# Performance work log

Hardware: AMD Instinct MI355X
Metric: run time of the kernel (lower is better)

The kernel has to match this reference:

```python
import jax, jax.numpy as jnp
import numpy as np

N, E, C, K = 50000, 800000, 64, 8
D = C * K  # 512
NEG_SLOPE = 0.01  # torch leaky_relu default


def setup_inputs() -> dict:
    key = jax.random.key(0)
    ks = jax.random.split(key, 6)
    x = jax.random.normal(ks[0], (N, D), dtype=jnp.float32)
    edge_index = jax.random.randint(ks[1], (2, E), 0, N, dtype=jnp.int64)
    conv_W = jax.random.normal(ks[2], (K, C, C), dtype=jnp.float32) * (1.0 / np.sqrt(C))
    conv_b = jax.random.normal(ks[3], (K, C), dtype=jnp.float32) * 0.01
    W1 = jax.random.normal(ks[4], (D, D), dtype=jnp.float32) * (1.0 / np.sqrt(D))
    W2 = jax.random.normal(ks[5], (D, D), dtype=jnp.float32) * (1.0 / np.sqrt(D))
    return {"x": x, "edge_index": edge_index, "conv_W": conv_W,
            "conv_b": conv_b, "W1": W1, "W2": W2}


def _gcn_conv(xk, Wk, bk, src, dst, dinv, n):
    # PyG GCNConv: transform, then symmetric-normalized aggregation with self-loops,
    # then add bias.
    xt = xk @ Wk.T  # [N, C]
    norm = dinv[src] * dinv[dst]  # [E]
    agg = jax.ops.segment_sum(norm[:, None] * xt[src], dst, num_segments=n)
    agg = agg + (dinv * dinv)[:, None] * xt  # self-loop contribution
    return agg + bk


def reference(x, edge_index, conv_W, conv_b, W1, W2):
    n = x.shape[0]
    src, dst = edge_index[0], edge_index[1]
    # degree with self-loops (edge weight 1)
    deg = jax.ops.segment_sum(jnp.ones((E,), x.dtype), dst, num_segments=n) + 1.0
    dinv = deg ** -0.5
    xr = x.reshape(n, C, K)
    zs = [jax.nn.leaky_relu(_gcn_conv(xr[:, :, i], conv_W[i], conv_b[i], src, dst, dinv, n),
                            negative_slope=NEG_SLOPE)
          for i in range(K)]
    z = jnp.concatenate(zs, axis=1)  # [N, D]
    z = jax.nn.leaky_relu(z, negative_slope=NEG_SLOPE)
    # dropout is identity in eval mode (dr=12 is invalid for torch Dropout anyway)
    z_fc1 = z @ W1.T
    z_fc2 = z @ W2.T
    s = jnp.sum(z_fc1.T @ z_fc2, axis=0)  # [D]
    # softmax over axis 0 of a [1, D] tensor (as in the original code)
    gate = jax.nn.softmax((s / jnp.sqrt(jnp.asarray(D, x.dtype)))[None, :], axis=0)
    return z * gate
```

## Files before the change

kernel.cpp:

```cpp
#include <hip/hip_runtime.h>

#define NN 50000
#define EE 800000
#define KK 8
#define DD 512
#define CAP 64
#define TR_BLOCKS   ((NN + 31) / 32)
#define FILL_BLOCKS ((EE + 255) / 256)
#define LROW 520

typedef __attribute__((ext_vector_type(8))) short short8;
typedef __attribute__((ext_vector_type(4))) float f32x4;
typedef __attribute__((ext_vector_type(4))) unsigned u32x4;

__device__ __forceinline__ float leaky2(float v) {
    v = (v < 0.0f) ? 0.01f * v : v;
    v = (v < 0.0f) ? 0.01f * v : v;
    return v;
}

__device__ __forceinline__ unsigned short f2bf(float f) {
    unsigned u = __float_as_uint(f);
    u += 0x7fffu + ((u >> 16) & 1u);
    return (unsigned short)(u >> 16);
}
__device__ __forceinline__ float bf_lo(unsigned u) { return __uint_as_float(u << 16); }
__device__ __forceinline__ float bf_hi(unsigned u) { return __uint_as_float(u & 0xffff0000u); }

__device__ __forceinline__ void fma8(float acc[8], float w, u32x4 v) {
    acc[0] += w * bf_lo(v[0]); acc[1] += w * bf_hi(v[0]);
    acc[2] += w * bf_lo(v[1]); acc[3] += w * bf_hi(v[1]);
    acc[4] += w * bf_lo(v[2]); acc[5] += w * bf_hi(v[2]);
    acc[6] += w * bf_lo(v[3]); acc[7] += w * bf_hi(v[3]);
}

__global__ __launch_bounds__(256) void k_fill_transform(
        const int* __restrict__ ei, int* __restrict__ cursor,
        unsigned short* __restrict__ bw,
        const float* __restrict__ x, const float* __restrict__ W,
        unsigned short* __restrict__ xt) {
    __shared__ unsigned short lxT[32 * LROW];
    const int t = threadIdx.x;

    if (blockIdx.x >= TR_BLOCKS) {
        int e = (blockIdx.x - TR_BLOCKS) * 256 + t;
        if (e < EE) {
            int s = ei[e];
            int d = ei[EE + e];
            int p = atomicAdd(&cursor[d], 1);
            if (p < CAP) bw[(size_t)d * CAP + p] = (unsigned short)s;
        }
        return;
    }

    const int n0 = blockIdx.x * 32;

    const f32x4* x4 = (const f32x4*)x;
    #pragma unroll
    for (int i = 0; i < 16; i++) {
        int idx = i * 256 + t;
        int n = idx >> 7;
        int q = idx & 127;
        int n_eff = n0 + n; if (n_eff >= NN) n_eff = NN - 1;
        f32x4 v = __builtin_nontemporal_load(&x4[(size_t)n_eff * 128 + q]);
        int c = q >> 1;
        int k0 = (q & 1) * 4;
        unsigned short* p = &lxT[n * LROW + k0 * 64 + c];
        p[0] = f2bf(v[0]); p[64] = f2bf(v[1]); p[128] = f2bf(v[2]); p[192] = f2bf(v[3]);
    }
    __syncthreads();

    const int wv   = t >> 6;
    const int lane = t & 63;
    const int l15  = lane & 15;
    const int quad = lane >> 4;
    const f32x4 zero = {0.f, 0.f, 0.f, 0.f};
    const f32x4* W4 = (const f32x4*)W;

    #pragma unroll
    for (int kk = 0; kk < 2; kk++) {
        const int k = wv * 2 + kk;
        short8 afr[4][2];
        #pragma unroll
        for (int jt = 0; jt < 4; jt++)
            #pragma unroll
            for (int ks = 0; ks < 2; ks++) {
                int off = (k * 4096 + (jt * 16 + l15) * 64 + ks * 32 + quad * 8) >> 2;
                f32x4 wa = W4[off], wb = W4[off + 1];
                short8 f;
                f[0] = (short)f2bf(wa[0]); f[1] = (short)f2bf(wa[1]);
                f[2] = (short)f2bf(wa[2]); f[3] = (short)f2bf(wa[3]);
                f[4] = (short)f2bf(wb[0]); f[5] = (short)f2bf(wb[1]);
                f[6] = (short)f2bf(wb[2]); f[7] = (short)f2bf(wb[3]);
                afr[jt][ks] = f;
            }

        #pragma unroll
        for (int ng = 0; ng < 2; ng++) {
            short8 bfr[2];
            #pragma unroll
            for (int ks = 0; ks < 2; ks++)
                bfr[ks] = *(const short8*)&lxT[(ng * 16 + l15) * LROW + k * 64 + ks * 32 + quad * 8];
            f32x4 acc[4];
            #pragma unroll
            for (int jt = 0; jt < 4; jt++) {
                acc[jt] = zero;
                acc[jt] = __builtin_amdgcn_mfma_f32_16x16x32_bf16(afr[jt][0], bfr[0], acc[jt], 0, 0, 0);
                acc[jt] = __builtin_amdgcn_mfma_f32_16x16x32_bf16(afr[jt][1], bfr[1], acc[jt], 0, 0, 0);
            }
            const int row = ng * 16 + l15;
            #pragma unroll
            for (int jt = 0; jt < 4; jt++) {
                ushort4 h;
                h.x = f2bf(acc[jt][0]); h.y = f2bf(acc[jt][1]);
                h.z = f2bf(acc[jt][2]); h.w = f2bf(acc[jt][3]);
                *(ushort4*)&lxT[row * LROW + k * 64 + jt * 16 + quad * 4] = h;
            }
        }
    }
    __syncthreads();

    #pragma unroll
    for (int i = 0; i < 8; i++) {
        int idx = i * 256 + t;
        int row = idx >> 6;
        int col8 = (idx & 63) * 8;
        int node = n0 + row;
        if (node < NN) {
            u32x4 v = *(const u32x4*)&lxT[row * LROW + col8];
            *(u32x4*)&xt[(size_t)node * DD + col8] = v;
        }
    }
}

__global__ __launch_bounds__(256) void k_agg(const unsigned short* __restrict__ xt,
                                             const int* __restrict__ cursor,
                                             const unsigned short* __restrict__ bw,
                                             const float* __restrict__ bias,
                                             float* __restrict__ out) {
    const int n = __builtin_amdgcn_readfirstlane(blockIdx.x * 4 + (threadIdx.x >> 6));
    const int lane = threadIdx.x & 63;
    const int cnr = cursor[n];
    const float dn = rsqrtf((float)cnr + 1.0f);
    const int cn = cnr > CAP ? CAP : cnr;

    const u32x4* xt4 = (const u32x4*)xt;
    int bidx = (int)bw[(size_t)n * CAP + lane];
    int sidx = lane < cn ? bidx : 0;
    float wl = rsqrtf((float)cursor[sidx] + 1.0f);
    u32x4 a = xt4[((size_t)n << 6) + lane];

    float acc[8];
    acc[0] = dn * bf_lo(a[0]); acc[1] = dn * bf_hi(a[0]);
    acc[2] = dn * bf_lo(a[1]); acc[3] = dn * bf_hi(a[1]);
    acc[4] = dn * bf_lo(a[2]); acc[5] = dn * bf_hi(a[2]);
    acc[6] = dn * bf_lo(a[3]); acc[7] = dn * bf_hi(a[3]);

    #define WLANE(i) __uint_as_float(__builtin_amdgcn_readlane(__float_as_uint(wl), (i)))
    int i = 0;
    for (; i + 3 < cn; i += 4) {
        int s0 = __builtin_amdgcn_readlane(bidx, i);
        int s1 = __builtin_amdgcn_readlane(bidx, i + 1);
        int s2 = __builtin_amdgcn_readlane(bidx, i + 2);
        int s3 = __builtin_amdgcn_readlane(bidx, i + 3);
        u32x4 v0 = xt4[((size_t)s0 << 6) + lane];
        u32x4 v1 = xt4[((size_t)s1 << 6) + lane];
        u32x4 v2 = xt4[((size_t)s2 << 6) + lane];
        u32x4 v3 = xt4[((size_t)s3 << 6) + lane];
        __builtin_amdgcn_sched_barrier(0);
        fma8(acc, WLANE(i), v0); fma8(acc, WLANE(i + 1), v1);
        fma8(acc, WLANE(i + 2), v2); fma8(acc, WLANE(i + 3), v3);
    }
    if (i + 1 < cn) {
        int s0 = __builtin_amdgcn_readlane(bidx, i);
        int s1 = __builtin_amdgcn_readlane(bidx, i + 1);
        u32x4 v0 = xt4[((size_t)s0 << 6) + lane];
        u32x4 v1 = xt4[((size_t)s1 << 6) + lane];
        fma8(acc, WLANE(i), v0); fma8(acc, WLANE(i + 1), v1);
        i += 2;
    }
    if (i < cn) {
        int s0 = __builtin_amdgcn_readlane(bidx, i);
        u32x4 v0 = xt4[((size_t)s0 << 6) + lane];
        fma8(acc, WLANE(i), v0);
    }
    #undef WLANE

    const float4* b4 = (const float4*)bias;
    float4 b0 = b4[lane * 2], b1 = b4[lane * 2 + 1];
    f32x4 r0, r1;
    r0[0] = leaky2(dn * acc[0] + b0.x); r0[1] = leaky2(dn * acc[1] + b0.y);
    r0[2] = leaky2(dn * acc[2] + b0.z); r0[3] = leaky2(dn * acc[3] + b0.w);
    r1[0] = leaky2(dn * acc[4] + b1.x); r1[1] = leaky2(dn * acc[5] + b1.y);
    r1[2] = leaky2(dn * acc[6] + b1.z); r1[3] = leaky2(dn * acc[7] + b1.w);
    f32x4* o4 = (f32x4*)(out + (size_t)n * DD);
    __builtin_nontemporal_store(r0, o4 + lane * 2);
    __builtin_nontemporal_store(r1, o4 + lane * 2 + 1);
}

extern "C" void kernel_launch(void* const* d_in, const int* in_sizes, int n_in,
                              void* d_out, int out_size, void* d_ws, size_t ws_size,
                              hipStream_t stream) {
    const float* x  = (const float*)d_in[0];
    const int*   ei = (const int*)d_in[1];
    const float* W  = (const float*)d_in[2];
    const float* b  = (const float*)d_in[3];
    float* out = (float*)d_out;

    unsigned short* xt = (unsigned short*)d_ws;
    int* cursor = (int*)(xt + (size_t)NN * DD);
    unsigned short* bw = (unsigned short*)(cursor + NN);

    hipMemsetAsync(cursor, 0, NN * sizeof(int), stream);
    k_fill_transform<<<TR_BLOCKS + FILL_BLOCKS, 256, 0, stream>>>(ei, cursor, bw, x, W, xt);
    k_agg<<<NN / 4, 256, 0, stream>>>(xt, cursor, bw, b, out);
}
```

Baseline: 380.6 us.

## Fold edge bucketing into transform blocks with alternating phase order

The separate edge-fill blocks are removed; every transform block now also buckets 512 edges, each thread handling two edges read through int2 loads. Odd blocks do their edge atomics before the transform and even blocks after it, so atomic traffic overlaps with the MFMA and global-load work of other blocks. This cuts the grid from about 4.7k blocks to about 1.6k and shortens the tail of the edge phase. In exchange, each block runs longer and the per-thread atomic sequence is serialized with the transform.

```diff
diff --git a/kernel.cpp b/kernel.cpp
--- a/kernel.cpp
+++ b/kernel.cpp
@@ -5,8 +5,7 @@
 #define KK 8
 #define DD 512
 #define CAP 64
-#define TR_BLOCKS   ((NN + 31) / 32)
-#define FILL_BLOCKS ((EE + 255) / 256)
+#define TR_BLOCKS ((NN + 31) / 32)
 #define LROW 520
 
 typedef __attribute__((ext_vector_type(8))) short short8;
@@ -34,26 +33,36 @@
     acc[6] += w * bf_lo(v[3]); acc[7] += w * bf_hi(v[3]);
 }
 
-__global__ __launch_bounds__(256) void k_fill_transform(
+__device__ __forceinline__ void do_edges(const int* __restrict__ ei,
+                                         int* __restrict__ cursor,
+                                         unsigned short* __restrict__ bw,
+                                         int b, int t) {
+    int e0 = (b * 256 + t) * 2;
+    if (e0 < EE) {
+        int2 s2 = *(const int2*)&ei[e0];
+        int2 d2 = *(const int2*)&ei[EE + e0];
+        int p = atomicAdd(&cursor[d2.x], 1);
+        if (p < CAP) bw[(size_t)d2.x * CAP + p] = (unsigned short)s2.x;
+        if (e0 + 1 < EE) {
+            p = atomicAdd(&cursor[d2.y], 1);
+            if (p < CAP) bw[(size_t)d2.y * CAP + p] = (unsigned short)s2.y;
+        }
+    }
+}
+
+__global__ __launch_bounds__(256) void k_transform_fill(
         const int* __restrict__ ei, int* __restrict__ cursor,
         unsigned short* __restrict__ bw,
         const float* __restrict__ x, const float* __restrict__ W,
         unsigned short* __restrict__ xt) {
     __shared__ unsigned short lxT[32 * LROW];
     const int t = threadIdx.x;
-
-    if (blockIdx.x >= TR_BLOCKS) {
-        int e = (blockIdx.x - TR_BLOCKS) * 256 + t;
-        if (e < EE) {
-            int s = ei[e];
-            int d = ei[EE + e];
-            int p = atomicAdd(&cursor[d], 1);
-            if (p < CAP) bw[(size_t)d * CAP + p] = (unsigned short)s;
-        }
-        return;
-    }
-
-    const int n0 = blockIdx.x * 32;
+    const int b = blockIdx.x;
+    const bool edges_first = (b & 1);
+
+    if (edges_first) do_edges(ei, cursor, bw, b, t);
+
+    const int n0 = b * 32;
 
     const f32x4* x4 = (const f32x4*)x;
     #pragma unroll
@@ -131,6 +140,8 @@
             *(u32x4*)&xt[(size_t)node * DD + col8] = v;
         }
     }
+
+    if (!edges_first) do_edges(ei, cursor, bw, b, t);
 }
 
 __global__ __launch_bounds__(256) void k_agg(const unsigned short* __restrict__ xt,
@@ -212,6 +223,6 @@
     unsigned short* bw = (unsigned short*)(cursor + NN);
 
     hipMemsetAsync(cursor, 0, NN * sizeof(int), stream);
-    k_fill_transform<<<TR_BLOCKS + FILL_BLOCKS, 256, 0, stream>>>(ei, cursor, bw, x, W, xt);
+    k_transform_fill<<<TR_BLOCKS, 256, 0, stream>>>(ei, cursor, bw, x, W, xt);
     k_agg<<<NN / 4, 256, 0, stream>>>(xt, cursor, bw, b, out);
 }
```

Result: faster. 348.8 us, median of 2 (-8.4%).
